# Performance work log

Hardware: AMD Instinct MI355X
Metric: run time of the kernel (lower is better)

The kernel has to match this reference:

```python
import jax, jax.numpy as jnp
import numpy as np

IN_DIM = 1024
OUT_DIM = 1024
HIDDEN = 1024
T = 16384
R_MIN, R_MAX, MAX_PHASE = 0.9, 0.999, 6.28


@jax.vmap
def binary_operator_diag(q_i, q_j):
    A_i, b_i = q_i
    A_j, b_j = q_j
    return (A_j * A_i, A_j * b_i + b_j)


def setup_inputs() -> dict:
    key = jax.random.key(0)
    ks = jax.random.split(key, 8)
    inputs = jax.random.normal(ks[0], (T, IN_DIM), dtype=jnp.float32)
    # nu_log / theta_log per original initializers
    u1 = jax.random.uniform(ks[1], (HIDDEN,), dtype=jnp.float32)
    nu_log = jnp.log(-0.5 * jnp.log(u1 * (R_MAX ** 2 - R_MIN ** 2) + R_MIN ** 2))
    u2 = jax.random.uniform(ks[2], (HIDDEN,), dtype=jnp.float32)
    theta_log = jnp.log(MAX_PHASE * u2)
    diag_lambda = jnp.exp(-jnp.exp(nu_log) + 1j * jnp.exp(theta_log))
    gamma_log = jnp.log(jnp.sqrt(1 - jnp.abs(diag_lambda) ** 2))
    B_re = jax.random.normal(ks[3], (IN_DIM, HIDDEN), dtype=jnp.float32) / jnp.sqrt(2.0 * IN_DIM)
    B_im = jax.random.normal(ks[4], (IN_DIM, HIDDEN), dtype=jnp.float32) / jnp.sqrt(2.0 * IN_DIM)
    C_re = jax.random.normal(ks[5], (OUT_DIM, HIDDEN), dtype=jnp.float32) / jnp.sqrt(1.0 * HIDDEN)
    C_im = jax.random.normal(ks[6], (OUT_DIM, HIDDEN), dtype=jnp.float32) / jnp.sqrt(1.0 * HIDDEN)
    D = jax.random.normal(ks[7], (OUT_DIM, IN_DIM), dtype=jnp.float32)
    return {"inputs": inputs, "nu_log": nu_log, "theta_log": theta_log,
            "gamma_log": gamma_log, "B_re": B_re, "B_im": B_im,
            "C_re": C_re, "C_im": C_im, "D": D}


def reference(inputs, nu_log, theta_log, gamma_log, B_re, B_im, C_re, C_im, D):
    # diagonal complex transition eigenvalues, shape (H,)
    diag_lambda = jnp.exp(-jnp.exp(nu_log) + 1j * jnp.exp(theta_log))
    # NOTE: original code expands gamma on axis=-1 -> (H, 1); broadcasts against
    # B_norm (in_dim, H) because in_dim == hidden_dim. Reproduced faithfully.
    B_norm = (B_re + 1j * B_im) * jnp.exp(gamma_log)[:, None]
    C = C_re + 1j * C_im
    T_len = inputs.shape[-2]
    Lambda_elements = jnp.repeat(diag_lambda[None, :], T_len, axis=0)  # (T, H)
    Bu_elements = jnp.einsum('ih,ti->th', B_norm, inputs)              # (T, H) complex
    _, hidden_states = jax.lax.associative_scan(
        binary_operator_diag, (Lambda_elements, Bu_elements))
    outputs = jnp.real(jnp.einsum('th,oh->to', hidden_states, C))      # (T, out)
    outputs = outputs + jnp.einsum('ti,io->to', inputs, D)             # D used as 'io'
    return outputs
```

## Files before the change

### kernel.cpp

```cpp
#include <hip/hip_runtime.h>
#include <hip/hip_bf16.h>
#include <stdint.h>

#define T_LEN   16384
#define HID     1024
#define KDIM    1024
#define CHUNK   64
#define NCHUNK  256

typedef __bf16 bf16x8 __attribute__((ext_vector_type(8)));
typedef float  f32x4  __attribute__((ext_vector_type(4)));

__device__ inline ushort f2bf(float f) {
  union { float f; uint32_t u; } v; v.f = f;
  uint32_t r = v.u + 0x7FFF + ((v.u >> 16) & 1);
  return (ushort)(r >> 16);
}
__device__ inline float bf2f(ushort u) {
  union { uint32_t u; float f; } v; v.u = ((uint32_t)u) << 16;
  return v.f;
}

__device__ inline void gload16(const void* g, void* l) {
  __builtin_amdgcn_global_load_lds(
      (const __attribute__((address_space(1))) void*)g,
      (__attribute__((address_space(3))) void*)l, 16, 0, 0);
}

__global__ __launch_bounds__(256) void prep_kernel(
    const float* __restrict__ nu_log, const float* __restrict__ theta_log,
    const float* __restrict__ gamma_log,
    float* __restrict__ lam_re, float* __restrict__ lam_im, float* __restrict__ eg) {
  int h = blockIdx.x * 256 + threadIdx.x;
  if (h < HID) {
    float mag = expf(-expf(nu_log[h]));
    float th  = expf(theta_log[h]);
    lam_re[h] = mag * cosf(th);
    lam_im[h] = mag * sinf(th);
    eg[h]     = expf(gamma_log[h]);
  }
}

__global__ __launch_bounds__(256) void convX(
    const float* __restrict__ src, ushort* __restrict__ dst) {
  size_t i = ((size_t)blockIdx.x * 256 + threadIdx.x) * 4;
  float4 v = *(const float4*)(src + i);
  ushort4 o;
  o.x = f2bf(v.x); o.y = f2bf(v.y); o.z = f2bf(v.z); o.w = f2bf(v.w);
  *(ushort4*)(dst + i) = o;
}

__global__ __launch_bounds__(256) void weight_prep(
    const float* __restrict__ Bre, const float* __restrict__ Bim,
    const float* __restrict__ Cre, const float* __restrict__ Cim,
    const float* __restrict__ D,   const float* __restrict__ eg,
    ushort* __restrict__ BreT, ushort* __restrict__ BimT,
    ushort* __restrict__ CreB, ushort* __restrict__ CimB,
    ushort* __restrict__ DT) {
  __shared__ float tile[32][33];
  int z = blockIdx.z;
  if (z == 2 || z == 3) {
    const float* src = (z == 2) ? Cre : Cim;
    ushort* dst = (z == 2) ? CreB : CimB;
    float s = (z == 2) ? 1.0f : -1.0f;
    size_t base = ((size_t)blockIdx.y * 32 + (threadIdx.x >> 3)) * 1024 +
                  blockIdx.x * 32 + (threadIdx.x & 7) * 4;
    float4 v = *(const float4*)(src + base);
    ushort4 o;
    o.x = f2bf(v.x * s); o.y = f2bf(v.y * s);
    o.z = f2bf(v.z * s); o.w = f2bf(v.w * s);
    *(ushort4*)(dst + base) = o;
    return;
  }
  const float* src = (z == 0) ? Bre : (z == 1) ? Bim : D;
  ushort* dst = (z == 0) ? BreT : (z == 1) ? BimT : DT;
  bool scaled = (z < 2);
  int bx = blockIdx.x * 32;
  int by = blockIdx.y * 32;
  int tx = threadIdx.x & 31, ty = threadIdx.x >> 5;
#pragma unroll
  for (int r = 0; r < 32; r += 8)
    tile[ty + r][tx] = src[(size_t)(by + ty + r) * 1024 + bx + tx];
  __syncthreads();
  float sc = scaled ? eg[by + tx] : 1.0f;
#pragma unroll
  for (int r = 0; r < 32; r += 8)
    dst[(size_t)(bx + ty + r) * 1024 + by + tx] = f2bf(tile[tx][ty + r] * sc);
}


#define BAR()   __builtin_amdgcn_s_barrier()
#define SCH0()  __builtin_amdgcn_sched_barrier(0)
#define LGKM0() asm volatile("s_waitcnt lgkmcnt(0)")
#define VM4()   asm volatile("s_waitcnt vmcnt(4)")
#define VM0()   asm volatile("s_waitcnt vmcnt(0)")

#define STAGE_HALF(G, LDA, R0, K0, LT, HALF)                         \
  do {                                                               \
    _Pragma("unroll")                                                \
    for (int is_ = 0; is_ < 2; ++is_) {                              \
      int seg_ = w * 2 + is_;                                        \
      int gr_ = (R0) + (HALF) * 128 + seg_ * 8 + (l >> 3);           \
      int gc_ = (K0) + (((l & 7) ^ (l >> 3)) << 3);                  \
      gload16((G) + (size_t)gr_ * (LDA) + gc_,                       \
              (LT) + (HALF) * 8192 + seg_ * 512);                    \
    }                                                                \
  } while (0)

#define DS_A(QM, BUF)                                                \
  do {                                                               \
    _Pragma("unroll")                                                \
    for (int m_ = 0; m_ < 4; ++m_) {                                 \
      int r_ = (wr * 128 + ((QM) * 4 + m_) * 16 + lo) * 64;          \
      a[m_][0] = *(const bf16x8*)((BUF) + r_ + c0us);                \
      a[m_][1] = *(const bf16x8*)((BUF) + r_ + c1us);                \
    }                                                                \
  } while (0)

#define DS_B(QN, BUF, REG)                                           \
  do {                                                               \
    _Pragma("unroll")                                                \
    for (int n_ = 0; n_ < 2; ++n_) {                                 \
      int r_ = (wc * 64 + ((QN) * 2 + n_) * 16 + lo) * 64;           \
      REG[n_][0] = *(const bf16x8*)((BUF) + r_ + c0us);              \
      REG[n_][1] = *(const bf16x8*)((BUF) + r_ + c1us);              \
    }                                                                \
  } while (0)

#define MFMA_Q(QM, QN, REG)                                          \
  do {                                                               \
    __builtin_amdgcn_s_setprio(1);                                   \
    _Pragma("unroll")                                                \
    for (int m_ = 0; m_ < 4; ++m_)                                   \
      _Pragma("unroll")                                              \
      for (int n_ = 0; n_ < 2; ++n_) {                               \
        f32x4* ac_ = &acc[(QM) * 4 + m_][(QN) * 2 + n_];             \
        *ac_ = __builtin_amdgcn_mfma_f32_16x16x32_bf16(              \
            a[m_][0], REG[n_][0], *ac_, 0, 0, 0);                    \
        *ac_ = __builtin_amdgcn_mfma_f32_16x16x32_bf16(              \
            a[m_][1], REG[n_][1], *ac_, 0, 0, 0);                    \
      }                                                              \
    __builtin_amdgcn_s_setprio(0);                                   \
  } while (0)

__device__ __forceinline__ void gemm256_seg(
    const ushort* __restrict__ A, int lda, const ushort* __restrict__ B,
    ushort* lds, int row0, int col0,
    int w, int l, int wr, int wc, int lo, int q, int c0us, int c1us,
    f32x4 acc[8][4]) {
  ushort* A0 = lds;
  ushort* A1 = lds + 16384;
  ushort* B0 = lds + 32768;
  ushort* B1 = lds + 49152;
  bf16x8 a[4][2], bq0[2][2], bq1[2][2];
  STAGE_HALF(A, lda, row0, 0, A0, 0);
  STAGE_HALF(A, lda, row0, 0, A0, 1);
  STAGE_HALF(B, 1024, col0, 0, B0, 0);
  STAGE_HALF(B, 1024, col0, 0, B0, 1);
  STAGE_HALF(B, 1024, col0, 64, B1, 0);
  STAGE_HALF(B, 1024, col0, 64, B1, 1);
  VM4(); BAR(); SCH0();
  for (int i = 0; i < 8; ++i) {
    const int k1 = (2 * i + 1) * 64;
    const int k2 = (2 * i + 2) * 64;
    const int k3 = (2 * i + 3) * 64;
    const bool st2 = (i < 7);
    DS_A(0, A0); DS_B(0, B0, bq0);
    STAGE_HALF(A, lda, row0, k1, A1, 0);
    BAR(); LGKM0(); SCH0(); MFMA_Q(0, 0, bq0); BAR(); SCH0();
    DS_B(1, B0, bq1);
    STAGE_HALF(A, lda, row0, k1, A1, 1);
    BAR(); LGKM0(); SCH0(); MFMA_Q(0, 1, bq1); BAR(); SCH0();
    DS_A(1, A0);
    if (st2) STAGE_HALF(B, 1024, col0, k2, B0, 0);
    BAR(); LGKM0(); SCH0(); MFMA_Q(1, 0, bq0); BAR(); SCH0();
    if (st2) { STAGE_HALF(B, 1024, col0, k2, B0, 1); VM4(); } else { VM0(); }
    BAR(); LGKM0(); SCH0(); MFMA_Q(1, 1, bq1); BAR(); SCH0();
    DS_A(0, A1); DS_B(0, B1, bq0);
    if (st2) STAGE_HALF(A, lda, row0, k2, A0, 0);
    BAR(); LGKM0(); SCH0(); MFMA_Q(0, 0, bq0); BAR(); SCH0();
    DS_B(1, B1, bq1);
    if (st2) STAGE_HALF(A, lda, row0, k2, A0, 1);
    BAR(); LGKM0(); SCH0(); MFMA_Q(0, 1, bq1); BAR(); SCH0();
    DS_A(1, A1);
    if (st2) STAGE_HALF(B, 1024, col0, k3, B1, 0);
    BAR(); LGKM0(); SCH0(); MFMA_Q(1, 0, bq0); BAR(); SCH0();
    if (st2) { STAGE_HALF(B, 1024, col0, k3, B1, 1); VM4(); } else { VM0(); }
    BAR(); LGKM0(); SCH0(); MFMA_Q(1, 1, bq1); BAR(); SCH0();
  }
}

__global__ __launch_bounds__(512, 2) void gemm_bu(
    const ushort* __restrict__ A, const ushort* __restrict__ B,
    ushort* __restrict__ O) {
  __shared__ __align__(16) ushort lds[65536];
  const int tid = threadIdx.x;
  const int w = tid >> 6, l = tid & 63;
  const int wr = w >> 2, wc = w & 3;
  const int lo = l & 15, q = l >> 4;
  const int xorv = (lo & 7) << 4;
  const int c0us = ((q * 16) ^ xorv) >> 1;
  const int c1us = ((64 + q * 16) ^ xorv) >> 1;
  const int id = blockIdx.y * 64 + blockIdx.x;
  const int nwg = 64 * (int)gridDim.y;
  const int s = (id & 7) * (nwg >> 3) + (id >> 3);
  const int row0 = (s & 63) * 256, col0 = (s >> 6) * 256;
  f32x4 acc[8][4];
#pragma unroll
  for (int m = 0; m < 8; ++m)
#pragma unroll
    for (int n = 0; n < 4; ++n) acc[m][n] = (f32x4){0.f, 0.f, 0.f, 0.f};
  gemm256_seg(A, 1024, B, lds, row0, col0, w, l, wr, wc, lo, q, c0us, c1us, acc);
  const int rowb = row0 + wr * 128, colb = col0 + wc * 64;
#pragma unroll
  for (int m = 0; m < 8; ++m)
#pragma unroll
    for (int n = 0; n < 4; ++n) {
      int col = colb + n * 16 + lo;
#pragma unroll
      for (int r = 0; r < 4; ++r)
        O[(size_t)(rowb + m * 16 + q * 4 + r) * 2048 + col] = f2bf(acc[m][n][r]);
    }
}

__global__ __launch_bounds__(512, 2) void gemm3(
    const ushort* __restrict__ Hall,
    const ushort* __restrict__ CreB, const ushort* __restrict__ CimB,
    const ushort* __restrict__ X,    const ushort* __restrict__ DT,
    float* __restrict__ O) {
  __shared__ __align__(16) ushort lds[65536];
  const int tid = threadIdx.x;
  const int w = tid >> 6, l = tid & 63;
  const int wr = w >> 2, wc = w & 3;
  const int lo = l & 15, q = l >> 4;
  const int xorv = (lo & 7) << 4;
  const int c0us = ((q * 16) ^ xorv) >> 1;
  const int c1us = ((64 + q * 16) ^ xorv) >> 1;
  const int id = blockIdx.y * 64 + blockIdx.x;
  const int nwg = 64 * (int)gridDim.y;
  const int s = (id & 7) * (nwg >> 3) + (id >> 3);
  const int row0 = (s & 63) * 256, col0 = (s >> 6) * 256;
  f32x4 acc[8][4];
#pragma unroll
  for (int m = 0; m < 8; ++m)
#pragma unroll
    for (int n = 0; n < 4; ++n) acc[m][n] = (f32x4){0.f, 0.f, 0.f, 0.f};
  gemm256_seg(Hall,        2048, CreB, lds, row0, col0, w, l, wr, wc, lo, q, c0us, c1us, acc);
  gemm256_seg(Hall + 1024, 2048, CimB, lds, row0, col0, w, l, wr, wc, lo, q, c0us, c1us, acc);
  gemm256_seg(X,           1024, DT,   lds, row0, col0, w, l, wr, wc, lo, q, c0us, c1us, acc);
  const int rowb = row0 + wr * 128, colb = col0 + wc * 64;
#pragma unroll
  for (int m = 0; m < 8; ++m)
#pragma unroll
    for (int n = 0; n < 4; ++n) {
      int col = colb + n * 16 + lo;
#pragma unroll
      for (int r = 0; r < 4; ++r)
        O[(size_t)(rowb + m * 16 + q * 4 + r) * HID + col] = acc[m][n][r];
    }
}

__global__ __launch_bounds__(256) void scan_sums(
    const ushort* __restrict__ Bu,
    const float* __restrict__ lam_re, const float* __restrict__ lam_im,
    float* __restrict__ Sre, float* __restrict__ Sim) {
  int h0 = (blockIdx.y * 256 + threadIdx.x) * 2;
  int c = blockIdx.x;
  float lr0 = lam_re[h0], li0 = lam_im[h0];
  float lr1 = lam_re[h0 + 1], li1 = lam_im[h0 + 1];
  float hr0 = 0.f, hi0 = 0.f, hr1 = 0.f, hi1 = 0.f;
  const uint* P = (const uint*)Bu;
  size_t baseR = (size_t)c * CHUNK * 1024 + (h0 >> 1);
  size_t baseI = baseR + 512;
#pragma unroll 8
  for (int t = 0; t < CHUNK; ++t) {
    uint re = P[baseR + (size_t)t * 1024];
    uint im = P[baseI + (size_t)t * 1024];
    float br0 = bf2f((ushort)re), br1 = bf2f((ushort)(re >> 16));
    float bi0 = bf2f((ushort)im), bi1 = bf2f((ushort)(im >> 16));
    float nr0 = fmaf(lr0, hr0, fmaf(-li0, hi0, br0));
    float ni0 = fmaf(lr0, hi0, fmaf(li0, hr0, bi0));
    float nr1 = fmaf(lr1, hr1, fmaf(-li1, hi1, br1));
    float ni1 = fmaf(lr1, hi1, fmaf(li1, hr1, bi1));
    hr0 = nr0; hi0 = ni0; hr1 = nr1; hi1 = ni1;
  }
  Sre[(size_t)c * HID + h0] = hr0;  Sre[(size_t)c * HID + h0 + 1] = hr1;
  Sim[(size_t)c * HID + h0] = hi0;  Sim[(size_t)c * HID + h0 + 1] = hi1;
}

__global__ __launch_bounds__(256) void scan_carry(
    const float* __restrict__ Sre, const float* __restrict__ Sim,
    const float* __restrict__ lam_re, const float* __restrict__ lam_im,
    float* __restrict__ Pre, float* __restrict__ Pim) {
  int h = blockIdx.x * 256 + threadIdx.x;
  float lr = lam_re[h], li = lam_im[h];
  float pr = lr, pi = li;
#pragma unroll
  for (int s = 0; s < 6; ++s) {
    float nr = pr * pr - pi * pi;
    float ni = 2.f * pr * pi;
    pr = nr; pi = ni;
  }
  float cr = 0.f, ci = 0.f;
  for (int c = 0; c < NCHUNK; ++c) {
    Pre[(size_t)c * HID + h] = cr;
    Pim[(size_t)c * HID + h] = ci;
    float sr = Sre[(size_t)c * HID + h];
    float si = Sim[(size_t)c * HID + h];
    float nr = fmaf(pr, cr, fmaf(-pi, ci, sr));
    float ni = fmaf(pr, ci, fmaf(pi, cr, si));
    cr = nr; ci = ni;
  }
}

__global__ __launch_bounds__(256) void scan_emit(
    const ushort* __restrict__ Bu,
    const float* __restrict__ lam_re, const float* __restrict__ lam_im,
    const float* __restrict__ Pre, const float* __restrict__ Pim,
    ushort* __restrict__ Hall) {
  int h0 = (blockIdx.y * 256 + threadIdx.x) * 2;
  int c = blockIdx.x;
  float lr0 = lam_re[h0], li0 = lam_im[h0];
  float lr1 = lam_re[h0 + 1], li1 = lam_im[h0 + 1];
  float hr0 = Pre[(size_t)c * HID + h0], hi0 = Pim[(size_t)c * HID + h0];
  float hr1 = Pre[(size_t)c * HID + h0 + 1], hi1 = Pim[(size_t)c * HID + h0 + 1];
  const uint* P = (const uint*)Bu;
  uint* Q = (uint*)Hall;
  size_t baseR = (size_t)c * CHUNK * 1024 + (h0 >> 1);
  size_t baseI = baseR + 512;
#pragma unroll 8
  for (int t = 0; t < CHUNK; ++t) {
    uint re = P[baseR + (size_t)t * 1024];
    uint im = P[baseI + (size_t)t * 1024];
    float br0 = bf2f((ushort)re), br1 = bf2f((ushort)(re >> 16));
    float bi0 = bf2f((ushort)im), bi1 = bf2f((ushort)(im >> 16));
    float nr0 = fmaf(lr0, hr0, fmaf(-li0, hi0, br0));
    float ni0 = fmaf(lr0, hi0, fmaf(li0, hr0, bi0));
    float nr1 = fmaf(lr1, hr1, fmaf(-li1, hi1, br1));
    float ni1 = fmaf(lr1, hi1, fmaf(li1, hr1, bi1));
    hr0 = nr0; hi0 = ni0; hr1 = nr1; hi1 = ni1;
    Q[baseR + (size_t)t * 1024] = (uint)f2bf(hr0) | ((uint)f2bf(hr1) << 16);
    Q[baseI + (size_t)t * 1024] = (uint)f2bf(hi0) | ((uint)f2bf(hi1) << 16);
  }
}

extern "C" void kernel_launch(void* const* d_in, const int* in_sizes, int n_in,
                              void* d_out, int out_size, void* d_ws, size_t ws_size,
                              hipStream_t stream) {
  const float* inputs    = (const float*)d_in[0];
  const float* nu_log    = (const float*)d_in[1];
  const float* theta_log = (const float*)d_in[2];
  const float* gamma_log = (const float*)d_in[3];
  const float* B_re      = (const float*)d_in[4];
  const float* B_im      = (const float*)d_in[5];
  const float* C_re      = (const float*)d_in[6];
  const float* C_im      = (const float*)d_in[7];
  const float* D         = (const float*)d_in[8];
  float* out = (float*)d_out;

  char* ws = (char*)d_ws;
  constexpr size_t TH = (size_t)T_LEN * HID;
  constexpr size_t W  = (size_t)1024 * 1024;
  constexpr size_t CH = (size_t)NCHUNK * HID;

  ushort* Xbf  = (ushort*)(ws);
  ushort* Bu   = (ushort*)(ws + TH * 2);
  ushort* Hall = (ushort*)(ws + TH * 6);
  char*   p    = ws + TH * 10;
  ushort* Ball = (ushort*)(p);             p += 2 * W * 2;
  ushort* CreB = (ushort*)(p);             p += W * 2;
  ushort* CimB = (ushort*)(p);             p += W * 2;
  ushort* DT   = (ushort*)(p);             p += W * 2;
  float*  Sre  = (float*)(p);              p += CH * 4;
  float*  Sim  = (float*)(p);              p += CH * 4;
  float*  Pre  = (float*)(p);              p += CH * 4;
  float*  Pim  = (float*)(p);              p += CH * 4;
  float*  lamR = (float*)(p);              p += 4096;
  float*  lamI = (float*)(p);              p += 4096;
  float*  eg   = (float*)(p);              p += 4096;
  ushort* BreT = Ball;
  ushort* BimT = Ball + W;

  prep_kernel<<<dim3(HID / 256), 256, 0, stream>>>(nu_log, theta_log, gamma_log,
                                                   lamR, lamI, eg);
  convX<<<dim3((unsigned)(TH / 4 / 256)), 256, 0, stream>>>(inputs, Xbf);
  weight_prep<<<dim3(32, 32, 5), 256, 0, stream>>>(B_re, B_im, C_re, C_im, D, eg,
                                                   BreT, BimT, CreB, CimB, DT);

  gemm_bu<<<dim3(T_LEN / 256, 2048 / 256), 512, 0, stream>>>(Xbf, Ball, Bu);

  scan_sums<<<dim3(NCHUNK, HID / 512), 256, 0, stream>>>(Bu, lamR, lamI, Sre, Sim);
  scan_carry<<<dim3(HID / 256), 256, 0, stream>>>(Sre, Sim, lamR, lamI, Pre, Pim);
  scan_emit<<<dim3(NCHUNK, HID / 512), 256, 0, stream>>>(Bu, lamR, lamI, Pre, Pim,
                                                         Hall);

  gemm3<<<dim3(T_LEN / 256, HID / 256), 512, 0, stream>>>(Hall, CreB, CimB, Xbf, DT,
                                                          out);
}
```

Baseline: 361.6 us.

## Rewrite GEMM main loop as register double-buffered pipeline across segments

Replaces the GEMM inner loop with a pipeline that double-buffers A/B fragments in registers (a0/a1, b0/b1). It drops explicit lgkmcnt waits and sched barriers, and prefetches the next segment's first tiles during the last iteration of the current one, so the three gemm3 segments run without pipeline drain. It also moves to a 1D grid with an explicit XCD-aware tile mapping, aimed at better L2 locality. It leaves an unused duplicate template, and removing the LDS waits and sched barriers depends on compiler-inserted waits for correctness and ordering.

After: 567.1 us. 56.9% more time.

```diff
diff --git a/kernel.cpp b/kernel.cpp
--- a/kernel.cpp
+++ b/kernel.cpp
@@ -90,10 +90,8 @@
 
 
 #define BAR()   __builtin_amdgcn_s_barrier()
-#define SCH0()  __builtin_amdgcn_sched_barrier(0)
-#define LGKM0() asm volatile("s_waitcnt lgkmcnt(0)")
-#define VM4()   asm volatile("s_waitcnt vmcnt(4)")
-#define VM0()   asm volatile("s_waitcnt vmcnt(0)")
+#define SETP(x) __builtin_amdgcn_s_setprio(x)
+#define VMW(N)  asm volatile("s_waitcnt vmcnt(" #N ")" ::: "memory")
 
 #define STAGE_HALF(G, LDA, R0, K0, LT, HALF)                         \
   do {                                                               \
@@ -107,86 +105,201 @@
     }                                                                \
   } while (0)
 
-#define DS_A(QM, BUF)                                                \
+#define DS_A(DST, BUF, QM)                                           \
   do {                                                               \
     _Pragma("unroll")                                                \
     for (int m_ = 0; m_ < 4; ++m_) {                                 \
-      int r_ = (wr * 128 + ((QM) * 4 + m_) * 16 + lo) * 64;          \
-      a[m_][0] = *(const bf16x8*)((BUF) + r_ + c0us);                \
-      a[m_][1] = *(const bf16x8*)((BUF) + r_ + c1us);                \
+      int r_ = (wr * 128 + (QM) * 64 + m_ * 16 + lo) * 64;           \
+      DST[m_][0] = *(const bf16x8*)((BUF) + r_ + c0us);              \
+      DST[m_][1] = *(const bf16x8*)((BUF) + r_ + c1us);              \
     }                                                                \
   } while (0)
 
-#define DS_B(QN, BUF, REG)                                           \
+#define DS_B(DST, BUF, QN)                                           \
   do {                                                               \
     _Pragma("unroll")                                                \
     for (int n_ = 0; n_ < 2; ++n_) {                                 \
-      int r_ = (wc * 64 + ((QN) * 2 + n_) * 16 + lo) * 64;           \
-      REG[n_][0] = *(const bf16x8*)((BUF) + r_ + c0us);              \
-      REG[n_][1] = *(const bf16x8*)((BUF) + r_ + c1us);              \
+      int r_ = (wc * 64 + (QN) * 32 + n_ * 16 + lo) * 64;            \
+      DST[n_][0] = *(const bf16x8*)((BUF) + r_ + c0us);              \
+      DST[n_][1] = *(const bf16x8*)((BUF) + r_ + c1us);              \
     }                                                                \
   } while (0)
 
-#define MFMA_Q(QM, QN, REG)                                          \
+#define MFMA_Q(QM, QN, AR, BR)                                       \
   do {                                                               \
-    __builtin_amdgcn_s_setprio(1);                                   \
+    SETP(1);                                                         \
     _Pragma("unroll")                                                \
     for (int m_ = 0; m_ < 4; ++m_)                                   \
       _Pragma("unroll")                                              \
       for (int n_ = 0; n_ < 2; ++n_) {                               \
         f32x4* ac_ = &acc[(QM) * 4 + m_][(QN) * 2 + n_];             \
         *ac_ = __builtin_amdgcn_mfma_f32_16x16x32_bf16(              \
-            a[m_][0], REG[n_][0], *ac_, 0, 0, 0);                    \
+            AR[m_][0], BR[n_][0], *ac_, 0, 0, 0);                    \
         *ac_ = __builtin_amdgcn_mfma_f32_16x16x32_bf16(              \
-            a[m_][1], REG[n_][1], *ac_, 0, 0, 0);                    \
+            AR[m_][1], BR[n_][1], *ac_, 0, 0, 0);                    \
       }                                                              \
-    __builtin_amdgcn_s_setprio(0);                                   \
+    SETP(0);                                                         \
   } while (0)
 
-__device__ __forceinline__ void gemm256_seg(
-    const ushort* __restrict__ A, int lda, const ushort* __restrict__ B,
-    ushort* lds, int row0, int col0,
-    int w, int l, int wr, int wc, int lo, int q, int c0us, int c1us,
-    f32x4 acc[8][4]) {
+template<int NSEG>
+__device__ __forceinline__ void gemm256_pipe(
+    const ushort* const Aseg[], const int ldaseg[], const ushort* const Bseg[],
+    ushort* lds, int row0, int col0, int w, int l,
+    int wr, int wc, int lo, int c0us, int c1us, f32x4 (&acc)[8][4]) {
   ushort* A0 = lds;
   ushort* A1 = lds + 16384;
   ushort* B0 = lds + 32768;
   ushort* B1 = lds + 49152;
-  bf16x8 a[4][2], bq0[2][2], bq1[2][2];
-  STAGE_HALF(A, lda, row0, 0, A0, 0);
-  STAGE_HALF(A, lda, row0, 0, A0, 1);
-  STAGE_HALF(B, 1024, col0, 0, B0, 0);
-  STAGE_HALF(B, 1024, col0, 0, B0, 1);
-  STAGE_HALF(B, 1024, col0, 64, B1, 0);
-  STAGE_HALF(B, 1024, col0, 64, B1, 1);
-  VM4(); BAR(); SCH0();
-  for (int i = 0; i < 8; ++i) {
-    const int k1 = (2 * i + 1) * 64;
-    const int k2 = (2 * i + 2) * 64;
-    const int k3 = (2 * i + 3) * 64;
-    const bool st2 = (i < 7);
-    DS_A(0, A0); DS_B(0, B0, bq0);
-    STAGE_HALF(A, lda, row0, k1, A1, 0);
-    BAR(); LGKM0(); SCH0(); MFMA_Q(0, 0, bq0); BAR(); SCH0();
-    DS_B(1, B0, bq1);
-    STAGE_HALF(A, lda, row0, k1, A1, 1);
-    BAR(); LGKM0(); SCH0(); MFMA_Q(0, 1, bq1); BAR(); SCH0();
-    DS_A(1, A0);
-    if (st2) STAGE_HALF(B, 1024, col0, k2, B0, 0);
-    BAR(); LGKM0(); SCH0(); MFMA_Q(1, 0, bq0); BAR(); SCH0();
-    if (st2) { STAGE_HALF(B, 1024, col0, k2, B0, 1); VM4(); } else { VM0(); }
-    BAR(); LGKM0(); SCH0(); MFMA_Q(1, 1, bq1); BAR(); SCH0();
-    DS_A(0, A1); DS_B(0, B1, bq0);
-    if (st2) STAGE_HALF(A, lda, row0, k2, A0, 0);
-    BAR(); LGKM0(); SCH0(); MFMA_Q(0, 0, bq0); BAR(); SCH0();
-    DS_B(1, B1, bq1);
-    if (st2) STAGE_HALF(A, lda, row0, k2, A0, 1);
-    BAR(); LGKM0(); SCH0(); MFMA_Q(0, 1, bq1); BAR(); SCH0();
-    DS_A(1, A1);
-    if (st2) STAGE_HALF(B, 1024, col0, k3, B1, 0);
-    BAR(); LGKM0(); SCH0(); MFMA_Q(1, 0, bq0); BAR(); SCH0();
-    if (st2) { STAGE_HALF(B, 1024, col0, k3, B1, 1); VM4(); } else { VM0(); }
-    BAR(); LGKM0(); SCH0(); MFMA_Q(1, 1, bq1); BAR(); SCH0();
+  bf16x8 a0[4][2], a1[4][2], b0[2][2], b1[2][2];
+
+  {
+    const ushort* A = Aseg[0]; const int lda = ldaseg[0];
+    const ushort* B = Bseg[0];
+    STAGE_HALF(A, lda, row0, 0, A0, 0);
+    STAGE_HALF(A, lda, row0, 0, A0, 1);
+    STAGE_HALF(B, 1024, col0, 0, B0, 0);
+    STAGE_HALF(B, 1024, col0, 0, B0, 1);
+    STAGE_HALF(A, lda, row0, 64, A1, 0);
+    STAGE_HALF(A, lda, row0, 64, A1, 1);
+    VMW(4);
+    BAR();
+    DS_A(a0, A0, 0);
+    DS_B(b0, B0, 0);
+  }
+
+#pragma unroll
+  for (int s = 0; s < NSEG; ++s) {
+    const ushort* A = Aseg[s]; const int lda = ldaseg[s];
+    const ushort* B = Bseg[s];
+    const bool hn = (s + 1 < NSEG);
+    const ushort* An = hn ? Aseg[s + 1] : (const ushort*)0;
+    const int ldan = hn ? ldaseg[s + 1] : 0;
+    const ushort* Bn = hn ? Bseg[s + 1] : (const ushort*)0;
+#pragma unroll 1
+    for (int i = 0; i < 8; ++i) {
+      const bool t7 = (i == 7);
+      const bool st = (!t7) || hn;
+      const bool vlast = t7 && !hn;
+      const ushort* SA2 = t7 ? An : A; const int la2 = t7 ? ldan : lda;
+      const ushort* SB2 = t7 ? Bn : B;
+      const int k1 = (2 * i + 1) * 64;
+      const int k2 = t7 ? 0 : (2 * i + 2) * 64;
+      const int k3 = t7 ? 64 : (2 * i + 3) * 64;
+      DS_B(b1, B0, 1);
+      STAGE_HALF(B, 1024, col0, k1, B1, 0);
+      MFMA_Q(0, 0, a0, b0);
+      BAR();
+      DS_A(a1, A0, 1);
+      STAGE_HALF(B, 1024, col0, k1, B1, 1);
+      MFMA_Q(0, 1, a0, b1);
+      BAR();
+      if (st) { STAGE_HALF(SA2, la2, row0, k2, A0, 0); VMW(2); }
+      else    { VMW(0); }
+      MFMA_Q(1, 0, a1, b0);
+      BAR();
+      DS_A(a0, A1, 0);
+      DS_B(b0, B1, 0);
+      if (st) STAGE_HALF(SA2, la2, row0, k2, A0, 1);
+      MFMA_Q(1, 1, a1, b1);
+      BAR();
+      DS_B(b1, B1, 1);
+      if (st) STAGE_HALF(SB2, 1024, col0, k2, B0, 0);
+      MFMA_Q(0, 0, a0, b0);
+      BAR();
+      DS_A(a1, A1, 1);
+      if (st) STAGE_HALF(SB2, 1024, col0, k2, B0, 1);
+      MFMA_Q(0, 1, a1 , b1);
+      BAR();
+      if (st) { STAGE_HALF(SA2 , la2, row0, k3, A1, 0); VMW(2); }
+      else    { VMW(0); }
+      MFMA_Q(1, 0, a1, b0);
+      BAR();
+      if (!vlast) { DS_A(a0, A0, 0); DS_B(b0, B0, 0); }
+      if (st) STAGE_HALF(SA2, la2, row0, k3, A1, 1);
+      MFMA_Q(1, 1, a1, b1);
+      BAR();
+    }
+  }
+}
+
+template<int NSEG>
+__device__ __forceinline__ void gemm256_pipe_fixed(
+    const ushort* const Aseg[], const int ldaseg[], const ushort* const Bseg[],
+    ushort* lds, int row0, int col0, int w, int l,
+    int wr, int wc, int lo, int c0us, int c1us, f32x4 (&acc)[8][4]) {
+  ushort* A0 = lds;
+  ushort* A1 = lds + 16384;
+  ushort* B0 = lds + 32768;
+  ushort* B1 = lds + 49152;
+  bf16x8 a0[4][2], a1[4][2], b0[2][2], b1[2][2];
+
+  {
+    const ushort* A = Aseg[0]; const int lda = ldaseg[0];
+    const ushort* B = Bseg[0];
+    STAGE_HALF(A, lda, row0, 0, A0, 0);
+    STAGE_HALF(A, lda, row0, 0, A0, 1);
+    STAGE_HALF(B, 1024, col0, 0, B0, 0);
+    STAGE_HALF(B, 1024, col0, 0, B0, 1);
+    STAGE_HALF(A, lda, row0, 64, A1, 0);
+    STAGE_HALF(A, lda, row0, 64, A1, 1);
+    VMW(4);
+    BAR();
+    DS_A(a0, A0, 0);
+    DS_B(b0, B0, 0);
+  }
+
+#pragma unroll
+  for (int s = 0; s < NSEG; ++s) {
+    const ushort* A = Aseg[s]; const int lda = ldaseg[s];
+    const ushort* B = Bseg[s];
+    const bool hn = (s + 1 < NSEG);
+    const ushort* An = hn ? Aseg[s + 1] : (const ushort*)0;
+    const int ldan = hn ? ldaseg[s + 1] : 0;
+    const ushort* Bn = hn ? Bseg[s + 1] : (const ushort*)0;
+#pragma unroll 1
+    for (int i = 0; i < 8; ++i) {
+      const bool t7 = (i == 7);
+      const bool st = (!t7) || hn;
+      const bool vlast = t7 && !hn;
+      const ushort* SA2 = t7 ? An : A; const int la2 = t7 ? ldan : lda;
+      const ushort* SB2 = t7 ? Bn : B;
+      const int k1 = (2 * i + 1) * 64;
+      const int k2 = t7 ? 0 : (2 * i + 2) * 64;
+      const int k3 = t7 ? 64 : (2 * i + 3) * 64;
+      DS_B(b1, B0, 1);
+      STAGE_HALF(B, 1024, col0, k1, B1, 0);
+      MFMA_Q(0, 0, a0, b0);
+      BAR();
+      DS_A(a1, A0, 1);
+      STAGE_HALF(B, 1024, col0, k1, B1, 1);
+      MFMA_Q(0, 1, a0, b1);
+      BAR();
+      if (st) { STAGE_HALF(SA2, la2, row0, k2, A0, 0); VMW(2); }
+      else    { VMW(0); }
+      MFMA_Q(1, 0, a1, b0);
+      BAR();
+      DS_A(a0, A1, 0);
+      DS_B(b0, B1, 0);
+      if (st) STAGE_HALF(SA2, la2, row0, k2, A0, 1);
+      MFMA_Q(1, 1, a1, b1);
+      BAR();
+      DS_B(b1, B1, 1);
+      if (st) STAGE_HALF(SB2, 1024, col0, k2, B0, 0);
+      MFMA_Q(0, 0, a0, b0);
+      BAR();
+      DS_A(a1, A1, 1);
+      if (st) STAGE_HALF(SB2, 1024, col0, k2, B0, 1);
+      MFMA_Q(0, 1, a0, b1);
+      BAR();
+      if (st) { STAGE_HALF(SA2, la2, row0, k3, A1, 0); VMW(2); }
+      else    { VMW(0); }
+      MFMA_Q(1, 0, a1, b0);
+      BAR();
+      if (!vlast) { DS_A(a0, A0, 0); DS_B(b0, B0, 0); }
+      if (st) STAGE_HALF(SA2, la2, row0, k3, A1, 1);
+      MFMA_Q(1, 1, a1, b1);
+      BAR();
+    }
   }
 }
 
@@ -201,16 +314,20 @@
   const int xorv = (lo & 7) << 4;
   const int c0us = ((q * 16) ^ xorv) >> 1;
   const int c1us = ((64 + q * 16) ^ xorv) >> 1;
-  const int id = blockIdx.y * 64 + blockIdx.x;
-  const int nwg = 64 * (int)gridDim.y;
-  const int s = (id & 7) * (nwg >> 3) + (id >> 3);
-  const int row0 = (s & 63) * 256, col0 = (s >> 6) * 256;
+  const int id = blockIdx.x;
+  const int xcd = id & 7, slot = id >> 3;
+  const int row0 = (xcd * 8 + (slot >> 3)) * 256;
+  const int col0 = (slot & 7) * 256;
   f32x4 acc[8][4];
 #pragma unroll
   for (int m = 0; m < 8; ++m)
 #pragma unroll
     for (int n = 0; n < 4; ++n) acc[m][n] = (f32x4){0.f, 0.f, 0.f, 0.f};
-  gemm256_seg(A, 1024, B, lds, row0, col0, w, l, wr, wc, lo, q, c0us, c1us, acc);
+  const ushort* Aseg[1] = {A};
+  const int     ldas[1] = {1024};
+  const ushort* Bseg[1] = {B};
+  gemm256_pipe_fixed<1>(Aseg, ldas, Bseg, lds, row0, col0, w, l, wr, wc, lo,
+                        c0us, c1us, acc);
   const int rowb = row0 + wr * 128, colb = col0 + wc * 64;
 #pragma unroll
   for (int m = 0; m < 8; ++m)
@@ -236,18 +353,20 @@
   const int xorv = (lo & 7) << 4;
   const int c0us = ((q * 16) ^ xorv) >> 1;
   const int c1us = ((64 + q * 16) ^ xorv) >> 1;
-  const int id = blockIdx.y * 64 + blockIdx.x;
-  const int nwg = 64 * (int)gridDim.y;
-  const int s = (id & 7) * (nwg >> 3) + (id >> 3);
-  const int row0 = (s & 63) * 256, col0 = (s >> 6) * 256;
+  const int id = blockIdx.x;
+  const int xcd = id & 7, slot = id >> 3;
+  const int row0 = (xcd * 8 + (slot >> 2)) * 256;
+  const int col0 = (slot & 3) * 256;
   f32x4 acc[8][4];
 #pragma unroll
   for (int m = 0; m < 8; ++m)
 #pragma unroll
     for (int n = 0; n < 4; ++n) acc[m][n] = (f32x4){0.f, 0.f, 0.f, 0.f};
-  gemm256_seg(Hall,        2048, CreB, lds, row0, col0, w, l, wr, wc, lo, q, c0us, c1us, acc);
-  gemm256_seg(Hall + 1024, 2048, CimB, lds, row0, col0, w, l, wr, wc, lo, q, c0us, c1us, acc);
-  gemm256_seg(X,           1024, DT,   lds, row0, col0, w, l, wr, wc, lo, q, c0us, c1us, acc);
+  const ushort* Aseg[3] = {Hall, Hall + 1024, X};
+  const int     ldas[3] = {2048, 2048, 1024};
+  const ushort* Bseg[3] = {CreB, CimB, DT};
+  gemm256_pipe_fixed<3>(Aseg, ldas, Bseg, lds, row0, col0, w, l, wr, wc, lo,
+                        c0us, c1us, acc);
   const int rowb = row0 + wr * 128, colb = col0 + wc * 64;
 #pragma unroll
   for (int m = 0; m < 8; ++m)
@@ -387,13 +506,12 @@
   weight_prep<<<dim3(32, 32, 5), 256, 0, stream>>>(B_re, B_im, C_re, C_im, D, eg,
                                                    BreT, BimT, CreB, CimB, DT);
 
-  gemm_bu<<<dim3(T_LEN / 256, 2048 / 256), 512, 0, stream>>>(Xbf, Ball, Bu);
+  gemm_bu<<<dim3(512), 512, 0, stream>>>(Xbf, Ball, Bu);
 
   scan_sums<<<dim3(NCHUNK, HID / 512), 256, 0, stream>>>(Bu, lamR, lamI, Sre, Sim);
   scan_carry<<<dim3(HID / 256), 256, 0, stream>>>(Sre, Sim, lamR, lamI, Pre, Pim);
   scan_emit<<<dim3(NCHUNK, HID / 512), 256, 0, stream>>>(Bu, lamR, lamI, Pre, Pim,
                                                          Hall);
 
-  gemm3<<<dim3(T_LEN / 256, HID / 256), 512, 0, stream>>>(Hall, CreB, CimB, Xbf, DT,
-                                                          out);
-}
+  gemm3<<<dim3(256), 512, 0, stream>>>(Hall, CreB, CimB, Xbf, DT, out);
+}
```
